# Kernel optimization log

Hardware: AMD Instinct MI355X
Metric: run time of the kernel (lower is better)

## Reference

```python
import jax, jax.numpy as jnp
import numpy as np
import math

N_HEADS = 16

def _layernorm(x, g, b):
    m = x.mean(-1, keepdims=True)
    v = ((x - m) ** 2).mean(-1, keepdims=True)
    return (x - m) * jax.lax.rsqrt(v + 1e-5) * g + b

def _project(x):
    # Poincare ball (c=1) projection: clip last-dim norm to 1 - eps
    max_norm = 1.0 - 1e-5
    n = jnp.linalg.norm(x, axis=-1, keepdims=True)
    return jnp.where(n > max_norm, x * (max_norm / jnp.maximum(n, 1e-12)), x)


def setup_inputs() -> dict:
    key = jax.random.key(0)
    ks = jax.random.split(key, 8)
    B, L, D = 2, 2048, 1024
    w = lambda k, s: jax.random.normal(k, s, jnp.float32) * 0.02
    return dict(
        x=jax.random.normal(ks[0], (B, L, D), jnp.float32),
        wq=w(ks[1], (D, D)), bq=jnp.zeros((D,), jnp.float32),
        wk=w(ks[2], (D, D)), bk=jnp.zeros((D,), jnp.float32),
        wv=w(ks[3], (D, D)), bv=jnp.zeros((D,), jnp.float32),
        wo=w(ks[4], (D, D)), bo=jnp.zeros((D,), jnp.float32),
        g1=jnp.ones((D,), jnp.float32), b1=jnp.zeros((D,), jnp.float32),
        g2=jnp.ones((D,), jnp.float32), b2=jnp.zeros((D,), jnp.float32),
        w1=w(ks[5], (4 * D, D)), bf1=jnp.zeros((4 * D,), jnp.float32),
        w2=w(ks[6], (D, 4 * D)), bf2=jnp.zeros((D,), jnp.float32),
    )


def reference(x, wq, bq, wk, bk, wv, bv, wo, bo, g1, b1, g2, b2, w1, bf1, w2, bf2):
    B, L, D = x.shape
    H = N_HEADS
    hd = D // H
    temp = math.sqrt(hd)

    xn = _layernorm(x, g1, b1)

    def heads(w, b):
        y = xn @ w.T + b                       # [B, L, D]
        return y.reshape(B, L, H, hd).transpose(0, 2, 1, 3)  # [B, H, L, hd]

    q = _project(heads(wq, bq))
    k = _project(heads(wk, bk))
    v = heads(wv, bv)

    # -||q - k||^2 / temp, via ||q||^2 + ||k||^2 - 2 q.k (same math as the
    # explicit broadcast-diff in the torch code, expressed as a GEMM)
    q2 = (q ** 2).sum(-1)[..., :, None]        # [B, H, L, 1]
    k2 = (k ** 2).sum(-1)[..., None, :]        # [B, H, 1, L]
    qk = jnp.einsum('bhld,bhmd->bhlm', q, k)   # [B, H, L, L]
    scores = -(q2 + k2 - 2.0 * qk) / temp
    attn = jax.nn.softmax(scores, axis=-1)     # dropout = identity (eval mode)

    out = jnp.einsum('bhlm,bhmd->bhld', attn, v)
    out = out.transpose(0, 2, 1, 3).reshape(B, L, D) @ wo.T + bo

    x = _project(x + out)
    xn2 = _layernorm(x, g2, b2)
    h = jax.nn.gelu(xn2 @ w1.T + bf1, approximate=False)  # torch nn.GELU = erf
    x = _project(x + (h @ w2.T + bf2))
    return x
```

## Files before the change

### kernel.cpp

```cpp
#include <hip/hip_runtime.h>
#include <math.h>

#define SEQ_L 2048
#define DM    1024
#define NH    16
#define HD    64
#define BL    4096
#define DFF   4096
#define QKV_S 3072

typedef __attribute__((ext_vector_type(8))) short short8;
typedef __attribute__((ext_vector_type(4))) short s16x4;
typedef __attribute__((ext_vector_type(4))) float f32x4;
typedef __attribute__((ext_vector_type(4))) int   i32x4;

#define C_QK  0.36067376022224085f
#define C_K2  0.18033688011112042f

#if __has_builtin(__builtin_amdgcn_exp2f)
#define EXP2(x) __builtin_amdgcn_exp2f(x)
#else
#define EXP2(x) exp2f(x)
#endif

__device__ __forceinline__ short f2bf(float x) {
    unsigned u = __float_as_uint(x);
    u += 0x7fff + ((u >> 16) & 1);
    return (short)(u >> 16);
}
__device__ __forceinline__ float bf2f(short s) {
    return __uint_as_float(((unsigned)(unsigned short)s) << 16);
}
__device__ __forceinline__ int cvt_pk_bf16(float lo, float hi) {
    int r;
    asm("v_cvt_pk_bf16_f32 %0, %1, %2" : "=v"(r) : "v"(lo), "v"(hi));
    return r;
}

__device__ __forceinline__ float gelu_fast(float x) {
    const float xa = fabsf(x);
    const float z = xa * 0.70710678118654752440f;
    const float t = __builtin_amdgcn_rcpf(fmaf(0.3275911f, z, 1.f));
    float P = fmaf(t, 1.061405429f, -1.453152027f);
    P = fmaf(t, P, 1.421413741f);
    P = fmaf(t, P, -0.284496736f);
    P = fmaf(t, P, 0.254829592f);
    P *= t;
    const float e = __expf(-z * z);
    const float erfp = fmaf(-P, e, 1.f);
    return 0.5f * fmaf(xa, erfp, x);
}

__device__ __forceinline__ float block_sum(float v, float* red, int tid) {
#pragma unroll
    for (int m = 32; m; m >>= 1) v += __shfl_xor(v, m);
    if ((tid & 63) == 0) red[tid >> 6] = v;
    __syncthreads();
    v = red[0] + red[1] + red[2] + red[3];
    __syncthreads();
    return v;
}

__global__ __launch_bounds__(256) void cvt6_kernel(
    const float* __restrict__ wq, const float* __restrict__ wk,
    const float* __restrict__ wv, const float* __restrict__ wo,
    const float* __restrict__ w1, const float* __restrict__ w2,
    short* __restrict__ dst) {
    const size_t i = (size_t)blockIdx.x * 256 + threadIdx.x;
    const float* src;
    size_t off;
    if (i < 1048576) {
        const int seg = (int)(i >> 18);
        off = i & 262143;
        src = seg == 0 ? wq : seg == 1 ? wk : seg == 2 ? wv : wo;
    } else if (i < 2097152) { src = w1; off = i - 1048576; }
    else                    { src = w2; off = i - 2097152; }
    const float4 v = ((const float4*)src)[off];
    const s16x4 o = {f2bf(v.x), f2bf(v.y), f2bf(v.z), f2bf(v.w)};
    ((s16x4*)dst)[i] = o;
}

__global__ __launch_bounds__(256) void ln_bf16_kernel(const float* __restrict__ x,
                                                      const float* __restrict__ g,
                                                      const float* __restrict__ b,
                                                      short* __restrict__ out) {
    const int row = blockIdx.x;
    const int tid = threadIdx.x;
    __shared__ float red[4];
    const float4 xv = *(const float4*)(x + (size_t)row * DM + tid * 4);
    float s = xv.x + xv.y + xv.z + xv.w;
    s = block_sum(s, red, tid);
    const float mean = s * (1.f / (float)DM);
    float dx0 = xv.x - mean, dx1 = xv.y - mean, dx2 = xv.z - mean, dx3 = xv.w - mean;
    float ss = dx0 * dx0 + dx1 * dx1 + dx2 * dx2 + dx3 * dx3;
    ss = block_sum(ss, red, tid);
    const float rs = 1.f / sqrtf(ss * (1.f / (float)DM) + 1e-5f);
    const float4 gv = *(const float4*)(g + tid * 4);
    const float4 bv = *(const float4*)(b + tid * 4);
    const s16x4 ob = {f2bf(dx0 * rs * gv.x + bv.x), f2bf(dx1 * rs * gv.y + bv.y),
                      f2bf(dx2 * rs * gv.z + bv.z), f2bf(dx3 * rs * gv.w + bv.w)};
    *(s16x4*)(out + (size_t)row * DM + tid * 4) = ob;
}

__global__ __launch_bounds__(256) void resproj_kernel(const float* __restrict__ a,
                                                      const float* __restrict__ c,
                                                      float* __restrict__ out) {
    const int row = blockIdx.x;
    const int tid = threadIdx.x;
    __shared__ float red[4];
    const float4 av = *(const float4*)(a + (size_t)row * DM + tid * 4);
    const float4 cv = *(const float4*)(c + (size_t)row * DM + tid * 4);
    float4 sv;
    sv.x = av.x + cv.x; sv.y = av.y + cv.y; sv.z = av.z + cv.z; sv.w = av.w + cv.w;
    float ss = sv.x * sv.x + sv.y * sv.y + sv.z * sv.z + sv.w * sv.w;
    ss = block_sum(ss, red, tid);
    const float n = sqrtf(ss);
    const float mx = 1.f - 1e-5f;
    const float scale = (n > mx) ? (mx / fmaxf(n, 1e-12f)) : 1.f;
    sv.x *= scale; sv.y *= scale; sv.z *= scale; sv.w *= scale;
    *(float4*)(out + (size_t)row * DM + tid * 4) = sv;
}

__global__ __launch_bounds__(256) void resproj2_kernel(const float* __restrict__ a,
                                                       const float* __restrict__ c0,
                                                       const float* __restrict__ c1,
                                                       float* __restrict__ out) {
    const int row = blockIdx.x;
    const int tid = threadIdx.x;
    __shared__ float red[4];
    const float4 av = *(const float4*)(a + (size_t)row * DM + tid * 4);
    const float4 cv = *(const float4*)(c0 + (size_t)row * DM + tid * 4);
    const float4 dv = *(const float4*)(c1 + (size_t)row * DM + tid * 4);
    float4 sv;
    sv.x = av.x + cv.x + dv.x; sv.y = av.y + cv.y + dv.y;
    sv.z = av.z + cv.z + dv.z; sv.w = av.w + cv.w + dv.w;
    float ss = sv.x * sv.x + sv.y * sv.y + sv.z * sv.z + sv.w * sv.w;
    ss = block_sum(ss, red, tid);
    const float n = sqrtf(ss);
    const float mx = 1.f - 1e-5f;
    const float scale = (n > mx) ? (mx / fmaxf(n, 1e-12f)) : 1.f;
    sv.x *= scale; sv.y *= scale; sv.z *= scale; sv.w *= scale;
    *(float4*)(out + (size_t)row * DM + tid * 4) = sv;
}

__global__ __launch_bounds__(256) void qk_prep(const short* __restrict__ qkvB,
                                               short* __restrict__ Qb,
                                               short* __restrict__ Kb,
                                               float* __restrict__ k2) {
    const int tid = threadIdx.x, lane = tid & 63;
    const int vec = blockIdx.x * 4 + (tid >> 6);
    const int row = vec >> 4, h = vec & 15;
    const int b = row >> 11, l = row & 2047;
    const size_t dstv = ((size_t)(b * NH + h) * SEQ_L + l) * HD + lane;
    const float mx = 1.f - 1e-5f;
    {
        const float v = bf2f(qkvB[(size_t)row * QKV_S + h * HD + lane]);
        float s = v * v;
#pragma unroll
        for (int m = 32; m; m >>= 1) s += __shfl_xor(s, m);
        const float n = sqrtf(s);
        const float sc = (n > mx) ? (mx / fmaxf(n, 1e-12f)) : 1.f;
        Qb[dstv] = f2bf(v * sc);
    }
    {
        const float v = bf2f(qkvB[(size_t)row * QKV_S + DM + h * HD + lane]);
        float s = v * v;
#pragma unroll
        for (int m = 32; m; m >>= 1) s += __shfl_xor(s, m);
        const float n = sqrtf(s);
        const float sc = (n > mx) ? (mx / fmaxf(n, 1e-12f)) : 1.f;
        Kb[dstv] = f2bf(v * sc);
        if (lane == 0) k2[(size_t)(b * NH + h) * SEQ_L + l] = s * sc * sc * C_K2;
    }
}

__global__ __launch_bounds__(256) void v_prep(const short* __restrict__ qkvB,
                                              short* __restrict__ Vtb) {
    const int blk = blockIdx.x;
    const int bh = blk >> 5, kt = blk & 31;
    const int b = bh >> 4, h = bh & 15;
    __shared__ short T[64 * 72];
    const int tid = threadIdx.x;
    {
        const int key = tid >> 2, ch = (tid & 3) * 16;
        const size_t src = ((size_t)b * SEQ_L + kt * 64 + key) * QKV_S + 2 * DM + h * HD + ch;
        *(short8*)&T[key * 72 + ch]     = *(const short8*)(qkvB + src);
        *(short8*)&T[key * 72 + ch + 8] = *(const short8*)(qkvB + src + 8);
    }
    __syncthreads();
    const int hd = tid >> 2, kc = (tid & 3) * 16;
    short8 o0, o1;
#pragma unroll
    for (int j = 0; j < 8; ++j) {
        o0[j] = T[(kc + j) * 72 + hd];
        o1[j] = T[(kc + 8 + j) * 72 + hd];
    }
    const int c32 = (kc >> 5) * 32;
    const int h4  = ((kc >> 4) & 1) * 4;
    short* dst = Vtb + ((size_t)bh * HD + hd) * SEQ_L + kt * 64 + c32 + h4;
    const s16x4 w0 = {o0[0], o0[1], o0[2], o0[3]};
    const s16x4 w1 = {o0[4], o0[5], o0[6], o0[7]};
    const s16x4 w2 = {o1[0], o1[1], o1[2], o1[3]};
    const s16x4 w3 = {o1[4], o1[5], o1[6], o1[7]};
    *(s16x4*)(dst)      = w0;
    *(s16x4*)(dst + 8)  = w1;
    *(s16x4*)(dst + 16) = w2;
    *(s16x4*)(dst + 24) = w3;
}

template <int BM, int ACT, int OUTBF, int FUSED, int SPLITK>
__global__ __launch_bounds__(256) void gemm_mfma(
    const short* __restrict__ A, const short* __restrict__ Bw,
    const float* __restrict__ bb0, const float* __restrict__ bb1,
    const float* __restrict__ bb2, void* __restrict__ Cout,
    void* __restrict__ Cout2,
    int M, int N, int K) {
    constexpr int RT = BM / 32;
    constexpr int LDSR = 40;
    constexpr bool VEPI = (OUTBF != 0) && (BM == 128);
    constexpr int STAGE_BYTES = (BM + 128) * LDSR * 2;
    constexpr int SMEM_BYTES = VEPI ? (4 * 64 * 72 * 2) : STAGE_BYTES;
    static_assert(!VEPI || SMEM_BYTES >= STAGE_BYTES, "VEPI smem too small");
    __shared__ __align__(16) char raw[SMEM_BYTES];
    short* As = (short*)raw;
    short* Bs = As + BM * LDSR;
    const int tid = threadIdx.x;
    const int wv = tid >> 6, lane = tid & 63;
    const int m0 = blockIdx.y * BM, n0 = blockIdx.x * 128;
    const int wr = (wv & 1) * (BM / 2);
    const int wc = (wv >> 1) * 64;

    const int z = (SPLITK > 1) ? blockIdx.z : 0;
    const int Kc = K / SPLITK;

    const int arow = wv * (BM / 4) + (lane >> 2);
    const int brow = wv * 32 + (lane >> 2);
    const short* Ag = A + (size_t)(m0 + arow) * K + z * Kc + (lane & 3) * 8;
    const short* Bg = Bw + (size_t)(n0 + brow) * K + z * Kc + (lane & 3) * 8;
    short* AsW = As + (wv * (BM / 4) + (lane >> 2)) * LDSR + (lane & 3) * 8;
    short* AsW2 = AsW + 16 * LDSR;
    short* BsW = Bs + (wv * 32 + (lane >> 2)) * LDSR + (lane & 3) * 8;
    short* BsW2 = BsW + 16 * LDSR;

    const f32x4 z4 = {0.f, 0.f, 0.f, 0.f};
    f32x4 acc[RT][4];
#pragma unroll
    for (int r = 0; r < RT; ++r)
#pragma unroll
        for (int c = 0; c < 4; ++c) acc[r][c] = z4;

    const int lrow = lane & 15, kq = (lane >> 4) * 8;

    short8 ra0, ra1, rb0, rb1;
    ra0 = *(const short8*)(Ag);
    if constexpr (BM == 128) ra1 = *(const short8*)(Ag + (size_t)16 * K);
    rb0 = *(const short8*)(Bg);
    rb1 = *(const short8*)(Bg + (size_t)16 * K);

    for (int kt = 0; kt < Kc; kt += 32) {
        __syncthreads();
        *(short8*)AsW = ra0;
        if constexpr (BM == 128) *(short8*)AsW2 = ra1;
        *(short8*)BsW = rb0;
        *(short8*)BsW2 = rb1;
        short8 na0, na1, nb0, nb1;
        if (kt + 32 < Kc) {
            na0 = *(const short8*)(Ag + kt + 32);
            if constexpr (BM == 128) na1 = *(const short8*)(Ag + (size_t)16 * K + kt + 32);
            nb0 = *(const short8*)(Bg + kt + 32);
            nb1 = *(const short8*)(Bg + (size_t)16 * K + kt + 32);
        }
        __syncthreads();
        short8 af[RT], bf[4];
#pragma unroll
        for (int r = 0; r < RT; ++r)
            af[r] = *(const short8*)&As[(wr + r * 16 + lrow) * LDSR + kq];
#pragma unroll
        for (int c = 0; c < 4; ++c)
            bf[c] = *(const short8*)&Bs[(wc + c * 16 + lrow) * LDSR + kq];
#pragma unroll
        for (int r = 0; r < RT; ++r)
#pragma unroll
            for (int c = 0; c < 4; ++c)
                acc[r][c] = __builtin_amdgcn_mfma_f32_16x16x32_bf16(af[r], bf[c], acc[r][c], 0, 0, 0);
        ra0 = na0; ra1 = na1; rb0 = nb0; rb1 = nb1;
    }

    void* Cbase = Cout;
    if constexpr (SPLITK > 1) { if (z) Cbase = Cout2; }

    const int col = lane & 15, rb = (lane >> 4) * 4;
    if constexpr (VEPI) {
        __syncthreads();
        short* Ot = (short*)raw + wv * (64 * 72);
#pragma unroll
        for (int c = 0; c < 4; ++c) {
            const int gn = n0 + wc + c * 16 + col;
            float bias;
            if constexpr (FUSED) {
                const int seg = gn >> 10;
                bias = (seg == 0 ? bb0 : seg == 1 ? bb1 : bb2)[gn & 1023];
            } else {
                bias = bb0[gn];
            }
#pragma unroll
            for (int r = 0; r < RT; ++r)
#pragma unroll
                for (int i = 0; i < 4; ++i) {
                    float v = acc[r][c][i] + bias;
                    if constexpr (ACT) v = gelu_fast(v);
                    Ot[(r * 16 + rb + i) * 72 + c * 16 + col] = f2bf(v);
                }
        }
        const int orow = lane >> 3, oc = (lane & 7) * 8;
#pragma unroll
        for (int it = 0; it < 8; ++it) {
            const short8 vv = *(const short8*)&Ot[(it * 8 + orow) * 72 + oc];
            *(short8*)((short*)Cbase + (size_t)(m0 + wr + it * 8 + orow) * N + n0 + wc + oc) = vv;
        }
    } else {
#pragma unroll
        for (int c = 0; c < 4; ++c) {
            const int gn = n0 + wc + c * 16 + col;
            float bias;
            if constexpr (FUSED) {
                const int seg = gn >> 10;
                bias = (seg == 0 ? bb0 : seg == 1 ? bb1 : bb2)[gn & 1023];
            } else {
                bias = bb0[gn];
            }
            if constexpr (SPLITK > 1) { if (z) bias = 0.f; }
#pragma unroll
            for (int r = 0; r < RT; ++r) {
                const int gm = m0 + wr + r * 16 + rb;
#pragma unroll
                for (int i = 0; i < 4; ++i) {
                    float v = acc[r][c][i] + bias;
                    if constexpr (ACT) v = gelu_fast(v);
                    if constexpr (OUTBF)
                        ((short*)Cbase)[(size_t)(gm + i) * N + gn] = f2bf(v);
                    else
                        ((float*)Cbase)[(size_t)(gm + i) * N + gn] = v;
                }
            }
        }
    }
}

__global__ __launch_bounds__(256) void attn_mfma2(const short* __restrict__ Qb,
                                                  const short* __restrict__ Kb,
                                                  const short* __restrict__ Vtb,
                                                  const float* __restrict__ k2v,
                                                  short* __restrict__ aO) {
    const int qt = blockIdx.x, h = blockIdx.y, b = blockIdx.z;
    const int tid = threadIdx.x, wv = tid >> 6, lane = tid & 63;
    const int bh = b * NH + h;
    constexpr int NT = SEQ_L / 64;
    constexpr int BUFS = 64 * 72;
    __shared__ __align__(16) short smem[4 * BUFS];
    __shared__ __align__(16) float k2s[SEQ_L];
    const int lrow = lane & 15, q8 = (lane >> 4) * 8, q4 = (lane >> 4) * 4;

    const short* Qh = Qb + (size_t)bh * SEQ_L * HD;
    const short* Kh = Kb + (size_t)bh * SEQ_L * HD;
    const short* Vh = Vtb + (size_t)bh * HD * SEQ_L;
    const float* k2p = k2v + (size_t)bh * SEQ_L;

    short8 qf[2][2];
#pragma unroll
    for (int nt = 0; nt < 2; ++nt)
#pragma unroll
        for (int kc = 0; kc < 2; ++kc)
            qf[nt][kc] = *(const short8*)(Qh +
                (size_t)(qt * 128 + wv * 32 + nt * 16 + lrow) * HD + kc * 32 + q8);

    {
        const float4 a0 = *(const float4*)(k2p + tid * 4);
        const float4 a1 = *(const float4*)(k2p + 1024 + tid * 4);
        *(float4*)&k2s[tid * 4] = a0;
        *(float4*)&k2s[1024 + tid * 4] = a1;
    }

    const int srow = tid >> 2, sch = (tid & 3) * 16;
    const short* gK = Kh + (size_t)srow * HD + sch;
    const short* gV = Vh + (size_t)srow * SEQ_L + sch;
    const int woff = srow * 72 + sch;

    {
        const short8 k0a = *(const short8*)(gK);
        const short8 k0b = *(const short8*)(gK + 8);
        const short8 v0a = *(const short8*)(gV);
        const short8 v0b = *(const short8*)(gV + 8);
        *(short8*)&smem[woff]            = k0a;
        *(short8*)&smem[woff + 8]        = k0b;
        *(short8*)&smem[BUFS + woff]     = v0a;
        *(short8*)&smem[BUFS + woff + 8] = v0b;
    }
    __syncthreads();

    const f32x4 z4 = {0.f, 0.f, 0.f, 0.f};
    f32x4 o[4][2];
#pragma unroll
    for (int ht = 0; ht < 4; ++ht)
#pragma unroll
        for (int nt = 0; nt < 2; ++nt) o[ht][nt] = z4;
    float lsum[2] = {0.f, 0.f};

    for (int kt = 0; kt < NT; ++kt) {
        const int k0 = kt * 64;
        const short* Ks = smem + (kt & 1) * (2 * BUFS);
        const short* Vt = Ks + BUFS;
        short8 nk0, nk1, nv0, nv1;
        const bool more = (kt + 1 < NT);
        if (more) {
            const short* g = gK + (size_t)(k0 + 64) * HD;
            nk0 = *(const short8*)(g);
            nk1 = *(const short8*)(g + 8);
            const short* gv2 = gV + (k0 + 64);
            nv0 = *(const short8*)(gv2);
            nv1 = *(const short8*)(gv2 + 8);
        }

        i32x4 pw[2][2];
#pragma unroll
        for (int mt = 0; mt < 4; ++mt) {
            const short8 kf0 = *(const short8*)&Ks[(mt * 16 + lrow) * 72 + q8];
            const short8 kf1 = *(const short8*)&Ks[(mt * 16 + lrow) * 72 + 32 + q8];
            const float4 kk = *(const float4*)&k2s[k0 + mt * 16 + q4];
            const int c = mt >> 1, wb = (mt & 1) * 2;
#pragma unroll
            for (int nt = 0; nt < 2; ++nt) {
                f32x4 s = z4;
                s = __builtin_amdgcn_mfma_f32_16x16x32_bf16(kf0, qf[nt][0], s, 0, 0, 0);
                s = __builtin_amdgcn_mfma_f32_16x16x32_bf16(kf1, qf[nt][1], s, 0, 0, 0);
                const float p0 = EXP2(fmaf(s[0], C_QK, -kk.x));
                const float p1 = EXP2(fmaf(s[1], C_QK, -kk.y));
                const float p2 = EXP2(fmaf(s[2], C_QK, -kk.z));
                const float p3 = EXP2(fmaf(s[3], C_QK, -kk.w));
                lsum[nt] += (p0 + p1) + (p2 + p3);
                pw[nt][c][wb]     = cvt_pk_bf16(p0, p1);
                pw[nt][c][wb + 1] = cvt_pk_bf16(p2, p3);
            }
        }
#pragma unroll
        for (int ht = 0; ht < 4; ++ht) {
#pragma unroll
            for (int c = 0; c < 2; ++c) {
                const short8 v8 = *(const short8*)&Vt[(ht * 16 + lrow) * 72 + c * 32 + q4 * 2];
#pragma unroll
                for (int nt = 0; nt < 2; ++nt)
                    o[ht][nt] = __builtin_amdgcn_mfma_f32_16x16x32_bf16(
                        v8, __builtin_bit_cast(short8, pw[nt][c]), o[ht][nt], 0, 0, 0);
            }
        }

        if (more) {
            short* Kd = smem + ((kt + 1) & 1) * (2 * BUFS);
            *(short8*)&Kd[woff]            = nk0;
            *(short8*)&Kd[woff + 8]        = nk1;
            *(short8*)&Kd[BUFS + woff]     = nv0;
            *(short8*)&Kd[BUFS + woff + 8] = nv1;
        }
        __syncthreads();
    }

#pragma unroll
    for (int nt = 0; nt < 2; ++nt) {
        lsum[nt] += __shfl_xor(lsum[nt], 16);
        lsum[nt] += __shfl_xor(lsum[nt], 32);
    }
    const float inv0 = 1.f / lsum[0], inv1 = 1.f / lsum[1];

    short* Ot = smem + wv * (32 * 72);
#pragma unroll
    for (int ht = 0; ht < 4; ++ht)
#pragma unroll
        for (int nt = 0; nt < 2; ++nt) {
            const float iv = nt ? inv1 : inv0;
            const s16x4 ov = {f2bf(o[ht][nt][0] * iv), f2bf(o[ht][nt][1] * iv),
                              f2bf(o[ht][nt][2] * iv), f2bf(o[ht][nt][3] * iv)};
            *(s16x4*)&Ot[(nt * 16 + lrow) * 72 + ht * 16 + q4] = ov;
        }
    const int erow = lane >> 1, ec = (lane & 1) * 32;
    const short8 r0 = *(const short8*)&Ot[erow * 72 + ec + 0];
    const short8 r1 = *(const short8*)&Ot[erow * 72 + ec + 8];
    const short8 r2 = *(const short8*)&Ot[erow * 72 + ec + 16];
    const short8 r3 = *(const short8*)&Ot[erow * 72 + ec + 24];
    short* dst = aO + ((size_t)b * SEQ_L + qt * 128 + wv * 32 + erow) * DM + h * HD + ec;
    *(short8*)(dst + 0)  = r0;
    *(short8*)(dst + 8)  = r1;
    *(short8*)(dst + 16) = r2;
    *(short8*)(dst + 24) = r3;
}

extern "C" void kernel_launch(void* const* d_in, const int* in_sizes, int n_in,
                              void* d_out, int out_size, void* d_ws, size_t ws_size,
                              hipStream_t stream) {
    const float* x   = (const float*)d_in[0];
    const float* wq  = (const float*)d_in[1];
    const float* bq  = (const float*)d_in[2];
    const float* wk  = (const float*)d_in[3];
    const float* bk  = (const float*)d_in[4];
    const float* wv  = (const float*)d_in[5];
    const float* bv  = (const float*)d_in[6];
    const float* wo  = (const float*)d_in[7];
    const float* bo  = (const float*)d_in[8];
    const float* g1  = (const float*)d_in[9];
    const float* b1  = (const float*)d_in[10];
    const float* g2  = (const float*)d_in[11];
    const float* b2  = (const float*)d_in[12];
    const float* w1  = (const float*)d_in[13];
    const float* bf1 = (const float*)d_in[14];
    const float* w2  = (const float*)d_in[15];
    const float* bf2 = (const float*)d_in[16];
    float* out = (float*)d_out;

    char* base = (char*)d_ws;
    short* wbf  = (short*)base;
    short* qkvB = (short*)(base + (24u << 20));
    short* xnb  = (short*)(base + (48u << 20));
    short* Qb   = xnb;
    short* Kb   = (short*)(base + (56u << 20));
    short* Vtb  = (short*)(base + (64u << 20));
    float* k2   = (float*)(base + (72u << 20));
    short* aO   = (short*)(base + (72u << 20) + (256u << 10));
    float* P    = (float*)(base + (24u << 20));
    float* P2   = (float*)(base + (40u << 20));
    short* xn2b = Vtb;
    short* hbuf = qkvB;
    float* y0   = (float*)base;
    float* y1   = (float*)(base + (56u << 20));

    cvt6_kernel<<<12288, 256, 0, stream>>>(wq, wk, wv, wo, w1, w2, wbf);
    ln_bf16_kernel<<<BL, 256, 0, stream>>>(x, g1, b1, xnb);
    gemm_mfma<128, 0, 1, 1, 1><<<dim3(24, 32), 256, 0, stream>>>(
        xnb, wbf, bq, bk, bv, qkvB, nullptr, BL, QKV_S, DM);
    qk_prep<<<16384, 256, 0, stream>>>(qkvB, Qb, Kb, k2);
    v_prep<<<1024, 256, 0, stream>>>(qkvB, Vtb);
    attn_mfma2<<<dim3(16, 16, 2), 256, 0, stream>>>(Qb, Kb, Vtb, k2, aO);
    gemm_mfma<128, 0, 0, 0, 2><<<dim3(8, 32, 2), 256, 0, stream>>>(
        aO, wbf + 3145728, bo, bo, bo, P, P2, BL, DM, DM);
    resproj2_kernel<<<BL, 256, 0, stream>>>(x, P, P2, out);
    ln_bf16_kernel<<<BL, 256, 0, stream>>>(out, g2, b2, xn2b);
    gemm_mfma<128, 1, 1, 0, 1><<<dim3(32, 32), 256, 0, stream>>>(
        xn2b, wbf + 4194304, bf1, bf1, bf1, hbuf, nullptr, BL, DFF, DM);
    gemm_mfma<128, 0, 0, 0, 2><<<dim3(8, 32, 2), 256, 0, stream>>>(
        hbuf, wbf + 8388608, bf2, bf2, bf2, y0, y1, BL, DM, DFF);
    resproj2_kernel<<<BL, 256, 0, stream>>>(out, y0, y1, out);
}
```

Baseline: 384.9 us.

## Double GEMM K-tile to 64 and remap workgroups across XCDs

The GEMM kernel now stages a 64-wide K slice per iteration instead of 32, using a new cooperative load pattern and a larger LDS tile. This halves the number of barrier pairs per K. Both the GEMM and attention kernels remap their linear workgroup IDs so that consecutive tiles land on the same XCD, which should improve L2 reuse of shared A/B rows and K/V heads. The cost is more LDS and registers per block, which may reduce occupancy. The attention remap hardcodes a 16x16x2 grid and breaks if those dimensions change.

```diff
diff --git a/kernel.cpp b/kernel.cpp
--- a/kernel.cpp
+++ b/kernel.cpp
@@ -215,32 +215,39 @@
     const float* __restrict__ bb2, void* __restrict__ Cout,
     void* __restrict__ Cout2,
     int M, int N, int K) {
+    static_assert(BM == 128, "BK=64 staging assumes BM=128");
     constexpr int RT = BM / 32;
-    constexpr int LDSR = 40;
+    constexpr int LDSR = 72;
     constexpr bool VEPI = (OUTBF != 0) && (BM == 128);
-    constexpr int STAGE_BYTES = (BM + 128) * LDSR * 2;
-    constexpr int SMEM_BYTES = VEPI ? (4 * 64 * 72 * 2) : STAGE_BYTES;
-    static_assert(!VEPI || SMEM_BYTES >= STAGE_BYTES, "VEPI smem too small");
-    __shared__ __align__(16) char raw[SMEM_BYTES];
-    short* As = (short*)raw;
-    short* Bs = As + BM * LDSR;
+    constexpr int STAGE_SHORTS = (BM + 128) * LDSR;
+    static_assert(!VEPI || STAGE_SHORTS >= 4 * 64 * 72, "VEPI smem too small");
+    __shared__ __align__(16) short raw[STAGE_SHORTS];
+    short* As = raw;
+    short* Bs = raw + BM * LDSR;
     const int tid = threadIdx.x;
     const int wv = tid >> 6, lane = tid & 63;
-    const int m0 = blockIdx.y * BM, n0 = blockIdx.x * 128;
+
+    const int gx = gridDim.x, gy = gridDim.y;
+    const int nwg = gx * gy * gridDim.z;
+    int d = blockIdx.x + gx * (blockIdx.y + gy * blockIdx.z);
+    d = (d & 7) * (nwg >> 3) + (d >> 3);
+    const int bx = d % gx;
+    const int byz = d / gx;
+    const int by = byz % gy;
+    const int bz = byz / gy;
+
+    const int m0 = by * BM, n0 = bx * 128;
     const int wr = (wv & 1) * (BM / 2);
     const int wc = (wv >> 1) * 64;
 
-    const int z = (SPLITK > 1) ? blockIdx.z : 0;
+    const int z = (SPLITK > 1) ? bz : 0;
     const int Kc = K / SPLITK;
 
-    const int arow = wv * (BM / 4) + (lane >> 2);
-    const int brow = wv * 32 + (lane >> 2);
-    const short* Ag = A + (size_t)(m0 + arow) * K + z * Kc + (lane & 3) * 8;
-    const short* Bg = Bw + (size_t)(n0 + brow) * K + z * Kc + (lane & 3) * 8;
-    short* AsW = As + (wv * (BM / 4) + (lane >> 2)) * LDSR + (lane & 3) * 8;
-    short* AsW2 = AsW + 16 * LDSR;
-    short* BsW = Bs + (wv * 32 + (lane >> 2)) * LDSR + (lane & 3) * 8;
-    short* BsW2 = BsW + 16 * LDSR;
+    const int srow = tid >> 3, sc8 = (tid & 7) * 8;
+    const short* Ag = A + (size_t)(m0 + srow) * K + z * Kc + sc8;
+    const short* Bg = Bw + (size_t)(n0 + srow) * K + z * Kc + sc8;
+    short* AsW = As + srow * LDSR + sc8;
+    short* BsW = Bs + srow * LDSR + sc8;
 
     const f32x4 z4 = {0.f, 0.f, 0.f, 0.f};
     f32x4 acc[RT][4];
@@ -251,48 +258,52 @@
 
     const int lrow = lane & 15, kq = (lane >> 4) * 8;
 
-    short8 ra0, ra1, rb0, rb1;
-    ra0 = *(const short8*)(Ag);
-    if constexpr (BM == 128) ra1 = *(const short8*)(Ag + (size_t)16 * K);
-    rb0 = *(const short8*)(Bg);
-    rb1 = *(const short8*)(Bg + (size_t)16 * K);
-
-    for (int kt = 0; kt < Kc; kt += 32) {
+    short8 ra[4], rb[4];
+#pragma unroll
+    for (int j = 0; j < 4; ++j) {
+        ra[j] = *(const short8*)(Ag + (size_t)(32 * j) * K);
+        rb[j] = *(const short8*)(Bg + (size_t)(32 * j) * K);
+    }
+
+    for (int kt = 0; kt < Kc; kt += 64) {
         __syncthreads();
-        *(short8*)AsW = ra0;
-        if constexpr (BM == 128) *(short8*)AsW2 = ra1;
-        *(short8*)BsW = rb0;
-        *(short8*)BsW2 = rb1;
-        short8 na0, na1, nb0, nb1;
-        if (kt + 32 < Kc) {
-            na0 = *(const short8*)(Ag + kt + 32);
-            if constexpr (BM == 128) na1 = *(const short8*)(Ag + (size_t)16 * K + kt + 32);
-            nb0 = *(const short8*)(Bg + kt + 32);
-            nb1 = *(const short8*)(Bg + (size_t)16 * K + kt + 32);
+#pragma unroll
+        for (int j = 0; j < 4; ++j) {
+            *(short8*)(AsW + (32 * j) * LDSR) = ra[j];
+            *(short8*)(BsW + (32 * j) * LDSR) = rb[j];
+        }
+        if (kt + 64 < Kc) {
+#pragma unroll
+            for (int j = 0; j < 4; ++j) {
+                ra[j] = *(const short8*)(Ag + (size_t)(32 * j) * K + kt + 64);
+                rb[j] = *(const short8*)(Bg + (size_t)(32 * j) * K + kt + 64);
+            }
         }
         __syncthreads();
-        short8 af[RT], bf[4];
-#pragma unroll
-        for (int r = 0; r < RT; ++r)
-            af[r] = *(const short8*)&As[(wr + r * 16 + lrow) * LDSR + kq];
-#pragma unroll
-        for (int c = 0; c < 4; ++c)
-            bf[c] = *(const short8*)&Bs[(wc + c * 16 + lrow) * LDSR + kq];
-#pragma unroll
-        for (int r = 0; r < RT; ++r)
+#pragma unroll
+        for (int h = 0; h < 2; ++h) {
+            short8 af[RT], bf[4];
+#pragma unroll
+            for (int r = 0; r < RT; ++r)
+                af[r] = *(const short8*)&As[(wr + r * 16 + lrow) * LDSR + h * 32 + kq];
 #pragma unroll
             for (int c = 0; c < 4; ++c)
-                acc[r][c] = __builtin_amdgcn_mfma_f32_16x16x32_bf16(af[r], bf[c], acc[r][c], 0, 0, 0);
-        ra0 = na0; ra1 = na1; rb0 = nb0; rb1 = nb1;
+                bf[c] = *(const short8*)&Bs[(wc + c * 16 + lrow) * LDSR + h * 32 + kq];
+#pragma unroll
+            for (int r = 0; r < RT; ++r)
+#pragma unroll
+                for (int c = 0; c < 4; ++c)
+                    acc[r][c] = __builtin_amdgcn_mfma_f32_16x16x32_bf16(af[r], bf[c], acc[r][c], 0, 0, 0);
+        }
     }
 
     void* Cbase = Cout;
     if constexpr (SPLITK > 1) { if (z) Cbase = Cout2; }
 
-    const int col = lane & 15, rb = (lane >> 4) * 4;
+    const int col = lane & 15, rb4 = (lane >> 4) * 4;
     if constexpr (VEPI) {
         __syncthreads();
-        short* Ot = (short*)raw + wv * (64 * 72);
+        short* Ot = raw + wv * (64 * 72);
 #pragma unroll
         for (int c = 0; c < 4; ++c) {
             const int gn = n0 + wc + c * 16 + col;
@@ -309,7 +320,7 @@
                 for (int i = 0; i < 4; ++i) {
                     float v = acc[r][c][i] + bias;
                     if constexpr (ACT) v = gelu_fast(v);
-                    Ot[(r * 16 + rb + i) * 72 + c * 16 + col] = f2bf(v);
+                    Ot[(r * 16 + rb4 + i) * 72 + c * 16 + col] = f2bf(v);
                 }
         }
         const int orow = lane >> 3, oc = (lane & 7) * 8;
@@ -332,7 +343,7 @@
             if constexpr (SPLITK > 1) { if (z) bias = 0.f; }
 #pragma unroll
             for (int r = 0; r < RT; ++r) {
-                const int gm = m0 + wr + r * 16 + rb;
+                const int gm = m0 + wr + r * 16 + rb4;
 #pragma unroll
                 for (int i = 0; i < 4; ++i) {
                     float v = acc[r][c][i] + bias;
@@ -352,7 +363,9 @@
                                                   const short* __restrict__ Vtb,
                                                   const float* __restrict__ k2v,
                                                   short* __restrict__ aO) {
-    const int qt = blockIdx.x, h = blockIdx.y, b = blockIdx.z;
+    int d = blockIdx.x + 16 * (blockIdx.y + 16 * blockIdx.z);
+    d = (d & 7) * 64 + (d >> 3);
+    const int qt = d & 15, h = (d >> 4) & 15, b = d >> 8;
     const int tid = threadIdx.x, wv = tid >> 6, lane = tid & 63;
     const int bh = b * NH + h;
     constexpr int NT = SEQ_L / 64;
```

Measured after the change: 378.8 us. Within noise of the previous version (-1.6%).
